# Kernel optimization log

Hardware: AMD Instinct MI355X
Metric: run time of the kernel (lower is better)

## Reference

```python
import jax, jax.numpy as jnp
import numpy as np

B, N, D, H = 8, 1024, 512, 8
DH = D // H  # one_head_dim = 64


def setup_inputs() -> dict:
    key = jax.random.key(0)
    ks = jax.random.split(key, 7)
    s = 0.02
    return {
        "x": jax.random.normal(ks[0], (B, N, D), dtype=jnp.float32),
        "bias": jax.random.normal(ks[1], (B, N, N, H), dtype=jnp.float32),
        "Wq": jax.random.normal(ks[2], (D, D), dtype=jnp.float32) * s,
        "Wk": jax.random.normal(ks[3], (D, D), dtype=jnp.float32) * s,
        "Wv": jax.random.normal(ks[4], (D, D), dtype=jnp.float32) * s,
        "Wm": jax.random.normal(ks[5], (D, D), dtype=jnp.float32) * s,
        "bm": jnp.zeros((D,), dtype=jnp.float32),
    }


def reference(x, bias, Wq, Wk, Wv, Wm, bm):
    # Linear layers (torch Linear: y = x @ W.T); dropout is identity at eval.
    scale = DH ** -0.5
    q = (x @ Wq.T).reshape(B, N, H, DH).transpose(0, 2, 1, 3) * scale  # [B,H,N,DH]
    k = (x @ Wk.T).reshape(B, N, H, DH).transpose(0, 2, 1, 3)
    v = (x @ Wv.T).reshape(B, N, H, DH).transpose(0, 2, 1, 3)
    # scores + additive pairwise bias (bias permuted [B,N,N,H] -> [B,H,N,N])
    scores = jnp.einsum("bhnd,bhmd->bhnm", q, k) + bias.transpose(0, 3, 1, 2)
    attn = jax.nn.softmax(scores, axis=-1)
    out = jnp.einsum("bhnm,bhmd->bhnd", attn, v)  # [B,H,N,DH]
    out = out.transpose(0, 2, 1, 3).reshape(B, N, D)
    return out @ Wm.T + bm
```

## Files before the change

### kernel.cpp

```cpp
#include <hip/hip_runtime.h>
#include <hip/hip_bf16.h>

typedef __bf16 bf16x8 __attribute__((ext_vector_type(8)));
typedef __bf16 bf16x4 __attribute__((ext_vector_type(4)));
typedef float  f32x4  __attribute__((ext_vector_type(4)));

#define MFMA16(a, b, c) __builtin_amdgcn_mfma_f32_16x16x32_bf16((a), (b), (c), 0, 0, 0)

typedef const __attribute__((address_space(1))) unsigned int* gas_t;
typedef __attribute__((address_space(3))) unsigned int* las_t;
__device__ __forceinline__ void dma16(const __bf16* g, __bf16* l) {
    __builtin_amdgcn_global_load_lds((gas_t)g, (las_t)l, 16, 0, 0);
}


__global__ __launch_bounds__(256) void gemm_qkv(
    const float* __restrict__ x,
    const float* __restrict__ Wq, const float* __restrict__ Wk,
    const float* __restrict__ Wv,
    __bf16* __restrict__ qo, __bf16* __restrict__ ko, __bf16* __restrict__ vto)
{
    __shared__ __bf16 As[128][40];
    __shared__ __bf16 Bs[128][40];
    const int tid  = threadIdx.x;
    const int lane = tid & 63;
    const int wid  = tid >> 6;
    const int g    = lane >> 4, l16 = lane & 15;
    const int wr   = wid >> 1,  wc  = wid & 1;
    const int r0   = blockIdx.x * 128;
    const int widx = blockIdx.y >> 2;
    const int c0   = (blockIdx.y & 3) * 128;
    const float* W = (widx == 0) ? Wq : (widx == 1 ? Wk : Wv);

    f32x4 acc[4][4] = {};

    for (int k0 = 0; k0 < 512; k0 += 32) {
        __syncthreads();
#pragma unroll
        for (int j = 0; j < 4; ++j) {
            const int idx = tid + 256 * j;
            const int r = idx >> 3, c4 = (idx & 7) * 4;
            f32x4 av = *reinterpret_cast<const f32x4*>(x + (size_t)(r0 + r) * 512 + k0 + c4);
            f32x4 bv = *reinterpret_cast<const f32x4*>(W + (size_t)(c0 + r) * 512 + k0 + c4);
            bf16x4 ap = { (__bf16)av.x, (__bf16)av.y, (__bf16)av.z, (__bf16)av.w };
            bf16x4 bp = { (__bf16)bv.x, (__bf16)bv.y, (__bf16)bv.z, (__bf16)bv.w };
            *reinterpret_cast<bf16x4*>(&As[r][c4]) = ap;
            *reinterpret_cast<bf16x4*>(&Bs[r][c4]) = bp;
        }
        __syncthreads();
        bf16x8 af[4], bfr[4];
#pragma unroll
        for (int i = 0; i < 4; ++i) {
            af[i]  = *reinterpret_cast<const bf16x8*>(&As[wr * 64 + i * 16 + l16][g * 8]);
            bfr[i] = *reinterpret_cast<const bf16x8*>(&Bs[wc * 64 + i * 16 + l16][g * 8]);
        }
#pragma unroll
        for (int i = 0; i < 4; ++i)
#pragma unroll
            for (int j = 0; j < 4; ++j)
                acc[i][j] = MFMA16(af[i], bfr[j], acc[i][j]);
    }

    if (widx == 2) {
#pragma unroll
        for (int rt = 0; rt < 4; ++rt)
#pragma unroll
            for (int ct = 0; ct < 4; ++ct) {
                int r = r0 + wr * 64 + rt * 16 + 4 * g;
                int c = c0 + wc * 64 + ct * 16 + l16;
                int b = r >> 10, n = r & 1023, h = c >> 6, dh = c & 63;
                bf16x4 pv = { (__bf16)acc[rt][ct][0], (__bf16)acc[rt][ct][1],
                              (__bf16)acc[rt][ct][2], (__bf16)acc[rt][ct][3] };
                size_t addr = (((size_t)(b * 8 + h) * 32 + (n >> 5)) * 64 + dh) * 32 + (n & 31);
                *reinterpret_cast<bf16x4*>(vto + addr) = pv;
            }
    } else {
        __bf16* dst = (widx == 0) ? qo : ko;
        const float scale = (widx == 0) ? 0.125f : 1.0f;
#pragma unroll
        for (int rt = 0; rt < 4; ++rt)
#pragma unroll
            for (int ct = 0; ct < 4; ++ct)
#pragma unroll
                for (int reg = 0; reg < 4; ++reg) {
                    int r = r0 + wr * 64 + rt * 16 + 4 * g + reg;
                    int c = c0 + wc * 64 + ct * 16 + l16;
                    float val = acc[rt][ct][reg] * scale;
                    int b = r >> 10, n = r & 1023, h = c >> 6, dh = c & 63;
                    dst[(((size_t)b * 8 + h) * 1024 + n) * 64 + dh] = (__bf16)val;
                }
    }
}

__global__ __launch_bounds__(512, 2) void attn_v13(
    const __bf16* __restrict__ qw, const __bf16* __restrict__ kw,
    const __bf16* __restrict__ vtw, const float* __restrict__ bias,
    __bf16* __restrict__ ow)
{
    __shared__ __align__(16) __bf16 Ks[8][32][64];
    __shared__ __align__(16) __bf16 Vs[8][64][32];
    __shared__ __align__(16) __bf16 bsm[2][8][32][36];
    __shared__ __bf16 psm[8][32][40];
    const int tid  = threadIdx.x;
    const int w    = tid >> 6;
    const int lane = tid & 63;
    const int g    = lane >> 4, l16 = lane & 15;
    const int b    = blockIdx.x;
    const int n0   = blockIdx.y * 32;
    const size_t bhs = (size_t)b * 8 + w;

    const __bf16* kbase  = kw  + bhs * 1024 * 64;
    const __bf16* vbase  = vtw + bhs * 32 * 2048;
    const float*  bias_b = bias + ((size_t)(b * 1024 + n0)) * 8192;

    const int snr = tid >> 4;
    const int sf  = tid & 15;

    const int k_row  = lane >> 3;
    const int k_csrc = (lane & 7) ^ (k_row & 7);
    const int v_dh   = lane >> 2;
    const int v_csrc = (lane & 3) ^ ((lane >> 3) & 3);
    const int v_rsw  = (l16 >> 1) & 3;

    bf16x8 qf[2][2];
#pragma unroll
    for (int rf = 0; rf < 2; ++rf)
#pragma unroll
        for (int kc = 0; kc < 2; ++kc)
            qf[rf][kc] = *reinterpret_cast<const bf16x8*>(
                qw + (bhs * 1024 + n0 + rf * 16 + l16) * 64 + kc * 32 + g * 8);

    f32x4 o[2][4] = {};
    float lrun[2][4] = {};

    f32x4 bpA[4], bpB[4];

#define LOAD_BIAS(dst, tt)                                                     \
    {                                                                          \
        const int m0_ = (tt) * 32;                                             \
        _Pragma("unroll")                                                      \
        for (int c = 0; c < 4; ++c)                                            \
            dst[c] = __builtin_nontemporal_load(reinterpret_cast<const f32x4*>(\
                bias_b + (size_t)snr * 8192 + m0_ * 8 + (sf + 16 * c) * 4));   \
    }

#define WRITE_BIAS(buf, src)                                                   \
    {                                                                          \
        _Pragma("unroll")                                                      \
        for (int c = 0; c < 4; ++c) {                                          \
            const int f4 = sf + 16 * c;                                        \
            const int mm = f4 >> 1, h0 = (f4 & 1) * 4;                         \
            bsm[buf][h0 + 0][mm][snr] = (__bf16)src[c].x;                      \
            bsm[buf][h0 + 1][mm][snr] = (__bf16)src[c].y;                      \
            bsm[buf][h0 + 2][mm][snr] = (__bf16)src[c].z;                      \
            bsm[buf][h0 + 3][mm][snr] = (__bf16)src[c].w;                      \
        }                                                                      \
    }

#define DMA_KV(tt)                                                             \
    {                                                                          \
        const int m0_ = (tt) * 32;                                             \
        _Pragma("unroll")                                                      \
        for (int i = 0; i < 4; ++i)                                            \
            dma16(kbase + (size_t)(m0_ + i * 8 + k_row) * 64 + k_csrc * 8,     \
                  &Ks[w][i * 8][0]);                                           \
        const __bf16* vblk = vbase + (size_t)(tt) * 2048;                      \
        _Pragma("unroll")                                                      \
        for (int i = 0; i < 4; ++i)                                            \
            dma16(vblk + (size_t)(i * 16 + v_dh) * 32 + v_csrc * 8,            \
                  &Vs[w][i * 16][0]);                                          \
    }

    LOAD_BIAS(bpA, 0)
    DMA_KV(0)
    WRITE_BIAS(0, bpA)
    LOAD_BIAS(bpA, 1)
    LOAD_BIAS(bpB, 2)
    asm volatile("s_waitcnt vmcnt(8)");
    __builtin_amdgcn_sched_barrier(0);
    asm volatile("s_waitcnt lgkmcnt(0)");
    __builtin_amdgcn_s_barrier();
    __builtin_amdgcn_sched_barrier(0);

#define ATTN_STEP(t, BUF, bpX)                                                 \
    {                                                                          \
        bf16x8 kf[2][2], vf[4];                                                \
        _Pragma("unroll")                                                      \
        for (int ct = 0; ct < 2; ++ct)                                         \
            _Pragma("unroll")                                                  \
            for (int kc = 0; kc < 2; ++kc) {                                   \
                const int mrow = ct * 16 + l16;                                \
                kf[ct][kc] = *reinterpret_cast<const bf16x8*>(                 \
                    &Ks[w][mrow][(((kc * 4 + g) ^ (l16 & 7)) * 8)]);           \
            }                                                                  \
        _Pragma("unroll")                                                      \
        for (int oc = 0; oc < 4; ++oc)                                         \
            vf[oc] = *reinterpret_cast<const bf16x8*>(                         \
                &Vs[w][oc * 16 + l16][(g ^ v_rsw) * 8]);                       \
        bf16x4 bb[2][2];                                                       \
        _Pragma("unroll")                                                      \
        for (int rf = 0; rf < 2; ++rf)                                         \
            _Pragma("unroll")                                                  \
            for (int ct = 0; ct < 2; ++ct)                                     \
                bb[rf][ct] = *reinterpret_cast<const bf16x4*>(                 \
                    &bsm[BUF][w][ct * 16 + l16][rf * 16 + 4 * g]);             \
                     \
        asm volatile("s_waitcnt lgkmcnt(0)");                                  \
        __builtin_amdgcn_sched_barrier(0);                                     \
        DMA_KV((t) + 1 < 32 ? (t) + 1 : 31)                                    \
        f32x4 s[2][2] = {};                                                    \
        __builtin_amdgcn_s_setprio(1);                                         \
        _Pragma("unroll")                                                      \
        for (int rf = 0; rf < 2; ++rf)                                         \
            _Pragma("unroll")                                                  \
            for (int ct = 0; ct < 2; ++ct) {                                   \
                s[rf][ct] = MFMA16(qf[rf][0], kf[ct][0], s[rf][ct]);           \
                s[rf][ct] = MFMA16(qf[rf][1], kf[ct][1], s[rf][ct]);           \
            }                                                                  \
        __builtin_amdgcn_s_setprio(0);                                         \
        _Pragma("unroll")                                                      \
        for (int rf = 0; rf < 2; ++rf)                                         \
            _Pragma("unroll")                                                  \
            for (int reg = 0; reg < 4; ++reg) {                                \
                const int nr = rf * 16 + 4 * g + reg;                          \
                float p0 = __expf(s[rf][0][reg] + (float)bb[rf][0][reg] - 16.0f); \
                float p1 = __expf(s[rf][1][reg] + (float)bb[rf][1][reg] - 16.0f); \
                lrun[rf][reg] += p0 + p1;                                      \
                psm[w][nr][l16]      = (__bf16)p0;                             \
                psm[w][nr][16 + l16] = (__bf16)p1;                             \
            }                                                                  \
        bf16x8 pf[2];                                                          \
        _Pragma("unroll")                                                      \
        for (int rf = 0; rf < 2; ++rf)                                         \
            pf[rf] = *reinterpret_cast<const bf16x8*>(&psm[w][rf * 16 + l16][g * 8]); \
        __builtin_amdgcn_s_setprio(1);                                         \
        _Pragma("unroll")                                                      \
        for (int rf = 0; rf < 2; ++rf)                                         \
            _Pragma("unroll")                                                  \
            for (int oc = 0; oc < 4; ++oc)                                     \
                o[rf][oc] = MFMA16(pf[rf], vf[oc], o[rf][oc]);                 \
        __builtin_amdgcn_s_setprio(0);                                         \
                        \
        WRITE_BIAS((BUF) ^ 1, bpX)                                             \
        LOAD_BIAS(bpX, (t) + 3 < 32 ? (t) + 3 : 31)                            \
                    \
        asm volatile("s_waitcnt vmcnt(4)");                                    \
        __builtin_amdgcn_sched_barrier(0);                                     \
        asm volatile("s_waitcnt lgkmcnt(0)");                                  \
        __builtin_amdgcn_s_barrier();                                          \
        __builtin_amdgcn_sched_barrier(0);                                     \
    }

    for (int t = 0; t < 32; t += 2) {
        ATTN_STEP(t,     0, bpA)
        ATTN_STEP(t + 1, 1, bpB)
    }
#undef ATTN_STEP
#undef LOAD_BIAS
#undef WRITE_BIAS
#undef DMA_KV

#pragma unroll
    for (int rf = 0; rf < 2; ++rf)
#pragma unroll
        for (int reg = 0; reg < 4; ++reg) {
            float l = lrun[rf][reg];
            l += __shfl_xor(l, 1);
            l += __shfl_xor(l, 2);
            l += __shfl_xor(l, 4);
            l += __shfl_xor(l, 8);
            lrun[rf][reg] = l;
        }

#pragma unroll
    for (int rf = 0; rf < 2; ++rf)
#pragma unroll
        for (int oc = 0; oc < 4; ++oc)
#pragma unroll
            for (int reg = 0; reg < 4; ++reg) {
                int n  = n0 + rf * 16 + 4 * g + reg;
                int dh = oc * 16 + l16;
                float val = o[rf][oc][reg] / lrun[rf][reg];
                ow[((size_t)b * 1024 + n) * 512 + w * 64 + dh] = (__bf16)val;
            }
}

__global__ __launch_bounds__(256) void gemm_out(
    const __bf16* __restrict__ a, const float* __restrict__ Wm,
    const float* __restrict__ bm, float* __restrict__ out)
{
    __shared__ __bf16 As[128][40];
    __shared__ __bf16 Bs[128][40];
    const int tid  = threadIdx.x;
    const int lane = tid & 63;
    const int wid  = tid >> 6;
    const int g    = lane >> 4, l16 = lane & 15;
    const int wr   = wid >> 1,  wc  = wid & 1;
    const int r0   = blockIdx.x * 128;
    const int c0   = blockIdx.y * 128;

    f32x4 acc[4][4] = {};

    for (int k0 = 0; k0 < 512; k0 += 32) {
        __syncthreads();
#pragma unroll
        for (int j = 0; j < 2; ++j) {
            const int idx = tid + 256 * j;
            const int r = idx >> 2, c8 = (idx & 3) * 8;
            bf16x8 av = *reinterpret_cast<const bf16x8*>(a + (size_t)(r0 + r) * 512 + k0 + c8);
            *reinterpret_cast<bf16x8*>(&As[r][c8]) = av;
        }
#pragma unroll
        for (int j = 0; j < 4; ++j) {
            const int idx = tid + 256 * j;
            const int r = idx >> 3, c4 = (idx & 7) * 4;
            f32x4 bv = *reinterpret_cast<const f32x4*>(Wm + (size_t)(c0 + r) * 512 + k0 + c4);
            bf16x4 bp = { (__bf16)bv.x, (__bf16)bv.y, (__bf16)bv.z, (__bf16)bv.w };
            *reinterpret_cast<bf16x4*>(&Bs[r][c4]) = bp;
        }
        __syncthreads();
        bf16x8 af[4], bfr[4];
#pragma unroll
        for (int i = 0; i < 4; ++i) {
            af[i]  = *reinterpret_cast<const bf16x8*>(&As[wr * 64 + i * 16 + l16][g * 8]);
            bfr[i] = *reinterpret_cast<const bf16x8*>(&Bs[wc * 64 + i * 16 + l16][g * 8]);
        }
#pragma unroll
        for (int i = 0; i < 4; ++i)
#pragma unroll
            for (int j = 0; j < 4; ++j)
                acc[i][j] = MFMA16(af[i], bfr[j], acc[i][j]);
    }

#pragma unroll
    for (int rt = 0; rt < 4; ++rt)
#pragma unroll
        for (int ct = 0; ct < 4; ++ct)
#pragma unroll
            for (int reg = 0; reg < 4; ++reg) {
                int r = r0 + wr * 64 + rt * 16 + 4 * g + reg;
                int c = c0 + wc * 64 + ct * 16 + l16;
                out[(size_t)r * 512 + c] = acc[rt][ct][reg] + bm[c];
            }
}

extern "C" void kernel_launch(void* const* d_in, const int* in_sizes, int n_in,
                              void* d_out, int out_size, void* d_ws, size_t ws_size,
                              hipStream_t stream)
{
    const float* x    = (const float*)d_in[0];
    const float* bias = (const float*)d_in[1];
    const float* Wq   = (const float*)d_in[2];
    const float* Wk   = (const float*)d_in[3];
    const float* Wv   = (const float*)d_in[4];
    const float* Wm   = (const float*)d_in[5];
    const float* bm   = (const float*)d_in[6];
    float* out = (float*)d_out;

    const size_t SEG = (size_t)8 * 8 * 1024 * 64;
    __bf16* qw  = (__bf16*)d_ws;
    __bf16* kw  = qw + SEG;
    __bf16* vtw = kw + SEG;
    __bf16* ow  = vtw + SEG;

    gemm_qkv<<<dim3(64, 12), 256, 0, stream>>>(x, Wq, Wk, Wv, qw, kw, vtw);
    attn_v13<<<dim3(8, 32), 512, 0, stream>>>(qw, kw, vtw, bias, ow);
    gemm_out<<<dim3(64, 4), 256, 0, stream>>>(ow, Wm, bm, out);
}
```

Baseline: 120.9 us.

## Double-buffer LDS and register-prefetch global loads in QKV and output GEMMs

Both projection GEMMs now use two LDS buffers plus register prefetch. The next tile is loaded from global memory into registers two steps ahead and written to the alternate LDS buffer while MFMAs run on the current one. This halves the barriers per k-step and replaces them with a barrier that only waits on LDS counters. The aim is to hide global load latency behind compute, at the cost of double the LDS footprint, more registers, and redundant clamped loads on the final steps.

```diff
diff --git a/kernel.cpp b/kernel.cpp
--- a/kernel.cpp
+++ b/kernel.cpp
@@ -11,6 +11,12 @@
 typedef __attribute__((address_space(3))) unsigned int* las_t;
 __device__ __forceinline__ void dma16(const __bf16* g, __bf16* l) {
     __builtin_amdgcn_global_load_lds((gas_t)g, (las_t)l, 16, 0, 0);
+}
+
+__device__ __forceinline__ void barrier_lds_only() {
+    asm volatile("s_waitcnt lgkmcnt(0)" ::: "memory");
+    __builtin_amdgcn_s_barrier();
+    __builtin_amdgcn_sched_barrier(0);
 }
 
 
@@ -20,8 +26,8 @@
     const float* __restrict__ Wv,
     __bf16* __restrict__ qo, __bf16* __restrict__ ko, __bf16* __restrict__ vto)
 {
-    __shared__ __bf16 As[128][40];
-    __shared__ __bf16 Bs[128][40];
+    __shared__ __bf16 As[2][128][40];
+    __shared__ __bf16 Bs[2][128][40];
     const int tid  = threadIdx.x;
     const int lane = tid & 63;
     const int wid  = tid >> 6;
@@ -33,33 +39,63 @@
     const float* W = (widx == 0) ? Wq : (widx == 1 ? Wk : Wv);
 
     f32x4 acc[4][4] = {};
-
-    for (int k0 = 0; k0 < 512; k0 += 32) {
-        __syncthreads();
-#pragma unroll
-        for (int j = 0; j < 4; ++j) {
-            const int idx = tid + 256 * j;
-            const int r = idx >> 3, c4 = (idx & 7) * 4;
-            f32x4 av = *reinterpret_cast<const f32x4*>(x + (size_t)(r0 + r) * 512 + k0 + c4);
-            f32x4 bv = *reinterpret_cast<const f32x4*>(W + (size_t)(c0 + r) * 512 + k0 + c4);
-            bf16x4 ap = { (__bf16)av.x, (__bf16)av.y, (__bf16)av.z, (__bf16)av.w };
-            bf16x4 bp = { (__bf16)bv.x, (__bf16)bv.y, (__bf16)bv.z, (__bf16)bv.w };
-            *reinterpret_cast<bf16x4*>(&As[r][c4]) = ap;
-            *reinterpret_cast<bf16x4*>(&Bs[r][c4]) = bp;
-        }
-        __syncthreads();
-        bf16x8 af[4], bfr[4];
-#pragma unroll
-        for (int i = 0; i < 4; ++i) {
-            af[i]  = *reinterpret_cast<const bf16x8*>(&As[wr * 64 + i * 16 + l16][g * 8]);
-            bfr[i] = *reinterpret_cast<const bf16x8*>(&Bs[wc * 64 + i * 16 + l16][g * 8]);
-        }
-#pragma unroll
-        for (int i = 0; i < 4; ++i)
-#pragma unroll
-            for (int j = 0; j < 4; ++j)
-                acc[i][j] = MFMA16(af[i], bfr[j], acc[i][j]);
-    }
+    f32x4 av[4], bv[4];
+
+#define QKV_LOAD(ks)                                                           \
+    {                                                                          \
+        const int k0_ = (ks) * 32;                                             \
+        _Pragma("unroll")                                                      \
+        for (int j = 0; j < 4; ++j) {                                          \
+            const int idx = tid + 256 * j;                                     \
+            const int r = idx >> 3, c4 = (idx & 7) * 4;                        \
+            av[j] = *reinterpret_cast<const f32x4*>(x + (size_t)(r0 + r) * 512 + k0_ + c4); \
+            bv[j] = *reinterpret_cast<const f32x4*>(W + (size_t)(c0 + r) * 512 + k0_ + c4); \
+        }                                                                      \
+    }
+
+#define QKV_WRITE(buf)                                                         \
+    {                                                                          \
+        _Pragma("unroll")                                                      \
+        for (int j = 0; j < 4; ++j) {                                          \
+            const int idx = tid + 256 * j;                                     \
+            const int r = idx >> 3, c4 = (idx & 7) * 4;                        \
+            bf16x4 ap = { (__bf16)av[j].x, (__bf16)av[j].y, (__bf16)av[j].z, (__bf16)av[j].w }; \
+            bf16x4 bp = { (__bf16)bv[j].x, (__bf16)bv[j].y, (__bf16)bv[j].z, (__bf16)bv[j].w }; \
+            *reinterpret_cast<bf16x4*>(&As[buf][r][c4]) = ap;                  \
+            *reinterpret_cast<bf16x4*>(&Bs[buf][r][c4]) = bp;                  \
+        }                                                                      \
+    }
+
+#define QKV_STEP(ks, BUF)                                                      \
+    {                                                                          \
+        bf16x8 af[4], bfr[4];                                                  \
+        _Pragma("unroll")                                                      \
+        for (int i = 0; i < 4; ++i) {                                          \
+            af[i]  = *reinterpret_cast<const bf16x8*>(&As[BUF][wr * 64 + i * 16 + l16][g * 8]); \
+            bfr[i] = *reinterpret_cast<const bf16x8*>(&Bs[BUF][wc * 64 + i * 16 + l16][g * 8]); \
+        }                                                                      \
+        _Pragma("unroll")                                                      \
+        for (int i = 0; i < 4; ++i)                                            \
+            _Pragma("unroll")                                                  \
+            for (int j = 0; j < 4; ++j)                                        \
+                acc[i][j] = MFMA16(af[i], bfr[j], acc[i][j]);                  \
+        QKV_WRITE((BUF) ^ 1)              \
+        QKV_LOAD((ks) + 2 < 16 ? (ks) + 2 : 15)                                \
+        barrier_lds_only();                                                    \
+    }
+
+    QKV_LOAD(0)
+    QKV_WRITE(0)
+    QKV_LOAD(1)
+    __syncthreads();
+
+    for (int ks = 0; ks < 16; ks += 2) {
+        QKV_STEP(ks,     0)
+        QKV_STEP(ks + 1, 1)
+    }
+#undef QKV_STEP
+#undef QKV_LOAD
+#undef QKV_WRITE
 
     if (widx == 2) {
 #pragma unroll
@@ -289,8 +325,8 @@
     const __bf16* __restrict__ a, const float* __restrict__ Wm,
     const float* __restrict__ bm, float* __restrict__ out)
 {
-    __shared__ __bf16 As[128][40];
-    __shared__ __bf16 Bs[128][40];
+    __shared__ __bf16 As[2][128][40];
+    __shared__ __bf16 Bs[2][128][40];
     const int tid  = threadIdx.x;
     const int lane = tid & 63;
     const int wid  = tid >> 6;
@@ -300,37 +336,73 @@
     const int c0   = blockIdx.y * 128;
 
     f32x4 acc[4][4] = {};
-
-    for (int k0 = 0; k0 < 512; k0 += 32) {
-        __syncthreads();
-#pragma unroll
-        for (int j = 0; j < 2; ++j) {
-            const int idx = tid + 256 * j;
-            const int r = idx >> 2, c8 = (idx & 3) * 8;
-            bf16x8 av = *reinterpret_cast<const bf16x8*>(a + (size_t)(r0 + r) * 512 + k0 + c8);
-            *reinterpret_cast<bf16x8*>(&As[r][c8]) = av;
-        }
-#pragma unroll
-        for (int j = 0; j < 4; ++j) {
-            const int idx = tid + 256 * j;
-            const int r = idx >> 3, c4 = (idx & 7) * 4;
-            f32x4 bv = *reinterpret_cast<const f32x4*>(Wm + (size_t)(c0 + r) * 512 + k0 + c4);
-            bf16x4 bp = { (__bf16)bv.x, (__bf16)bv.y, (__bf16)bv.z, (__bf16)bv.w };
-            *reinterpret_cast<bf16x4*>(&Bs[r][c4]) = bp;
-        }
-        __syncthreads();
-        bf16x8 af[4], bfr[4];
-#pragma unroll
-        for (int i = 0; i < 4; ++i) {
-            af[i]  = *reinterpret_cast<const bf16x8*>(&As[wr * 64 + i * 16 + l16][g * 8]);
-            bfr[i] = *reinterpret_cast<const bf16x8*>(&Bs[wc * 64 + i * 16 + l16][g * 8]);
-        }
-#pragma unroll
-        for (int i = 0; i < 4; ++i)
-#pragma unroll
-            for (int j = 0; j < 4; ++j)
-                acc[i][j] = MFMA16(af[i], bfr[j], acc[i][j]);
-    }
+    bf16x8 avp[2];
+    f32x4  bvp[4];
+
+#define OUT_LOAD(ks)                                                           \
+    {                                                                          \
+        const int k0_ = (ks) * 32;                                             \
+        _Pragma("unroll")                                                      \
+        for (int j = 0; j < 2; ++j) {                                          \
+            const int idx = tid + 256 * j;                                     \
+            const int r = idx >> 2, c8 = (idx & 3) * 8;                        \
+            avp[j] = *reinterpret_cast<const bf16x8*>(a + (size_t)(r0 + r) * 512 + k0_ + c8); \
+        }                                                                      \
+        _Pragma("unroll")                                                      \
+        for (int j = 0; j < 4; ++j) {                                          \
+            const int idx = tid + 256 * j;                                     \
+            const int r = idx >> 3, c4 = (idx & 7) * 4;                        \
+            bvp[j] = *reinterpret_cast<const f32x4*>(Wm + (size_t)(c0 + r) * 512 + k0_ + c4); \
+        }                                                                      \
+    }
+
+#define OUT_WRITE(buf)                                                         \
+    {                                                                          \
+        _Pragma("unroll")                                                      \
+        for (int j = 0; j < 2; ++j) {                                          \
+            const int idx = tid + 256 * j;                                     \
+            const int r = idx >> 2, c8 = (idx & 3) * 8;                        \
+            *reinterpret_cast<bf16x8*>(&As[buf][r][c8]) = avp[j];              \
+        }                                                                      \
+        _Pragma("unroll")                                                      \
+        for (int j = 0; j < 4; ++j) {                                          \
+            const int idx = tid + 256 * j;                                     \
+            const int r = idx >> 3, c4 = (idx & 7) * 4;                        \
+            bf16x4 bp = { (__bf16)bvp[j].x, (__bf16)bvp[j].y, (__bf16)bvp[j].z, (__bf16)bvp[j].w }; \
+            *reinterpret_cast<bf16x4*>(&Bs[buf][r][c4]) = bp;                  \
+        }                                                                      \
+    }
+
+#define OUT_STEP(ks, BUF)                                                      \
+    {                                                                          \
+        bf16x8 af[4], bfr[4];                                                  \
+        _Pragma("unroll")                                                      \
+        for (int i = 0; i < 4; ++i) {                                          \
+            af[i]  = *reinterpret_cast<const bf16x8*>(&As[BUF][wr * 64 + i * 16 + l16][g * 8]); \
+            bfr[i] = *reinterpret_cast<const bf16x8*>(&Bs[BUF][wc * 64 + i * 16 + l16][g * 8]); \
+        }                                                                      \
+        _Pragma("unroll")                                                      \
+        for (int i = 0; i < 4; ++i)                                            \
+            _Pragma("unroll")                                                  \
+            for (int j = 0; j < 4; ++j)                                        \
+                acc[i][j] = MFMA16(af[i], bfr[j], acc[i][j]);                  \
+        OUT_WRITE((BUF) ^ 1)                                                   \
+        OUT_LOAD((ks) + 2 < 16 ? (ks) + 2 : 15)                                \
+        barrier_lds_only();                                                    \
+    }
+
+    OUT_LOAD(0)
+    OUT_WRITE(0)
+    OUT_LOAD(1)
+    __syncthreads();
+
+    for (int ks = 0; ks < 16; ks += 2) {
+        OUT_STEP(ks,     0)
+        OUT_STEP(ks + 1, 1)
+    }
+#undef OUT_STEP
+#undef OUT_LOAD
+#undef OUT_WRITE
 
 #pragma unroll
     for (int rt = 0; rt < 4; ++rt)
```

After: 114.5 us. 5.2% less time.
